# Kernel tuning notes

Measured on AMD Instinct MI355X. Metric: run time of the kernel, lower is better.

The kernel has to match this reference:

```python
import jax, jax.numpy as jnp
import numpy as np

B, C, P, H, W = 64, 2048, 4, 14, 14
HID = C * P // 2  # 4096
S = H * W         # 196


def setup_inputs() -> dict:
    key = jax.random.key(0)
    k1, k2, k3, k4, k5 = jax.random.split(key, 5)
    x = jax.random.normal(k1, (B, C, H, W), dtype=jnp.float32)
    w1 = jax.random.normal(k2, (HID, C), dtype=jnp.float32) * 0.02
    b1 = jnp.zeros((HID,), dtype=jnp.float32)
    w2 = jax.random.normal(k3, (C * P, HID), dtype=jnp.float32) * 0.02
    b2 = jnp.zeros((C * P,), dtype=jnp.float32)
    return {"x": x, "w1": w1, "b1": b1, "w2": w2, "b2": b2}


def reference(x, w1, b1, w2, b2):
    # SE-style gating: global average pool -> fc1 -> sigmoid -> fc2 -> sigmoid
    g = x.mean(axis=(2, 3))                                  # [B, C]
    h = jax.nn.sigmoid(g @ w1.T + b1)                        # [B, HID]
    w = jax.nn.sigmoid(h @ w2.T + b2).reshape(B, P, C)       # grouping_result [B, P, C]
    # Weighted feature: mean over channels of w[b,p,c] * x[b,c,s].
    # Original materializes [B,P,C,196] then AdaptiveAvgPool3d over C;
    # mathematically this is a batched matmul divided by C.
    xs = x.reshape(B, C, S)                                  # [B, C, 196]
    feat = jnp.einsum('bpc,bcs->bps', w, xs) / C             # [B, P, 196]
    return (w, feat.reshape(B, P, H, W))
```

## Files before the change

### kernel.cpp

```cpp
#include <hip/hip_runtime.h>
#include <hip/hip_bf16.h>
#include <cstdint>
#include <cstddef>

typedef __attribute__((ext_vector_type(4))) float  f32x4;
typedef __attribute__((ext_vector_type(8))) short  short8;

typedef __attribute__((address_space(3))) uint32_t as3_u32;
typedef __attribute__((address_space(1))) uint32_t as1_u32;

__device__ __forceinline__ short f2bf(float f) {
  __hip_bfloat16 h = __float2bfloat16(f);
  return *reinterpret_cast<short*>(&h);
}
__device__ __forceinline__ float sigmoidf(float x) {
  return 1.0f / (1.0f + __expf(-x));
}

__global__ __launch_bounds__(256) void pool_kernel(const float* __restrict__ x,
                                                   short* __restrict__ g) {
  __shared__ float sums[784];
  const int tid = threadIdx.x;
  const f32x4* base = (const f32x4*)(x + (size_t)blockIdx.x * (16 * 196));
#pragma unroll
  for (int it = 0; it < 4; ++it) {
    int i = it * 256 + tid;
    if (it < 3 || tid < 16) {
      f32x4 v = base[i];
      sums[i] = v[0] + v[1] + v[2] + v[3];
    }
  }
  __syncthreads();
  if (tid < 16) {
    float s = 0.f;
#pragma unroll
    for (int j = 0; j < 49; ++j) s += sums[tid * 49 + j];
    g[blockIdx.x * 16 + tid] = f2bf(s * (1.0f / 196.0f));
  }
}

template<int N, int K, int WAVES, bool OUT_BF16>
__device__ __forceinline__ void gemm_body(const short* __restrict__ A,
                                          const float* __restrict__ B,
                                          const float* __restrict__ bias,
                                          void* __restrict__ outp,
                                          float* __restrict__ red) {
  constexpr int KW = K / WAVES;
  constexpr int NK = KW / 32;
  constexpr int NT = WAVES * 64;
  const int n0  = blockIdx.x * 16;
  const int tid = threadIdx.x;
  const int l   = tid & 63;
  const int wv  = tid >> 6;
  const int kw0 = wv * KW;

  const int ko = (l >> 4) * 8;
  const float* Bp = B + (size_t)(n0 + (l & 15)) * K + kw0 + ko;
  const short* Ap = A + (size_t)(l & 15) * K + kw0 + ko;

  f32x4 acc0 = {}, acc1 = {}, acc2 = {}, acc3 = {};

  f32x4 bc0 = *(const f32x4*)(Bp);
  f32x4 bc1 = *(const f32x4*)(Bp + 4);
  short8 ac0 = *(const short8*)(Ap);
  short8 ac1 = *(const short8*)(Ap + 16 * K);
  short8 ac2 = *(const short8*)(Ap + 32 * K);
  short8 ac3 = *(const short8*)(Ap + 48 * K);

  for (int t = 0; t < NK; ++t) {
    f32x4 bn0 = {}, bn1 = {};
    short8 an0 = {}, an1 = {}, an2 = {}, an3 = {};
    if (t + 1 < NK) {
      const float* bp = Bp + (t + 1) * 32;
      const short* ap = Ap + (t + 1) * 32;
      bn0 = *(const f32x4*)(bp);
      bn1 = *(const f32x4*)(bp + 4);
      an0 = *(const short8*)(ap);
      an1 = *(const short8*)(ap + 16 * K);
      an2 = *(const short8*)(ap + 32 * K);
      an3 = *(const short8*)(ap + 48 * K);
    }
    short8 bb;
    bb[0] = f2bf(bc0[0]); bb[1] = f2bf(bc0[1]); bb[2] = f2bf(bc0[2]); bb[3] = f2bf(bc0[3]);
    bb[4] = f2bf(bc1[0]); bb[5] = f2bf(bc1[1]); bb[6] = f2bf(bc1[2]); bb[7] = f2bf(bc1[3]);
    acc0 = __builtin_amdgcn_mfma_f32_16x16x32_bf16(ac0, bb, acc0, 0, 0, 0);
    acc1 = __builtin_amdgcn_mfma_f32_16x16x32_bf16(ac1, bb, acc1, 0, 0, 0);
    acc2 = __builtin_amdgcn_mfma_f32_16x16x32_bf16(ac2, bb, acc2, 0, 0, 0);
    acc3 = __builtin_amdgcn_mfma_f32_16x16x32_bf16(ac3, bb, acc3, 0, 0, 0);
    bc0 = bn0; bc1 = bn1;
    ac0 = an0; ac1 = an1; ac2 = an2; ac3 = an3;
  }

  {
    float* rw = red + wv * 1024;
    const int mb = (l >> 4) << 2;
    const int nn = l & 15;
#pragma unroll
    for (int r = 0; r < 4; ++r) rw[(0  + mb + r) * 16 + nn] = acc0[r];
#pragma unroll
    for (int r = 0; r < 4; ++r) rw[(16 + mb + r) * 16 + nn] = acc1[r];
#pragma unroll
    for (int r = 0; r < 4; ++r) rw[(32 + mb + r) * 16 + nn] = acc2[r];
#pragma unroll
    for (int r = 0; r < 4; ++r) rw[(48 + mb + r) * 16 + nn] = acc3[r];
  }
  __syncthreads();

#pragma unroll
  for (int i = tid; i < 1024; i += NT) {
    float s = 0.f;
#pragma unroll
    for (int w = 0; w < WAVES; ++w) s += red[w * 1024 + i];
    int m  = i >> 4;
    int nn = n0 + (i & 15);
    s = sigmoidf(s + bias[nn]);
    if constexpr (OUT_BF16) ((short*)outp)[(size_t)m * N + nn] = f2bf(s);
    else                    ((float*)outp)[(size_t)m * N + nn] = s;
  }
}

__global__ __launch_bounds__(1024, 4) void gemm1_kernel(const short* __restrict__ A,
                                                        const float* __restrict__ B,
                                                        const float* __restrict__ bias,
                                                        short* __restrict__ outp) {
  __shared__ float red[16 * 1024];
  gemm_body<4096, 2048, 16, true>(A, B, bias, outp, red);
}

__global__ __launch_bounds__(512, 4) void gemm2_kernel(const short* __restrict__ A,
                                                       const float* __restrict__ B,
                                                       const float* __restrict__ bias,
                                                       float* __restrict__ outp,
                                                       float* __restrict__ zbuf) {
  constexpr int N = 8192, K = 4096;
  __shared__ float lds[16384];
  const int tid = threadIdx.x;
  const int l   = tid & 63;
  const int wv  = tid >> 6;
  const int n0  = blockIdx.x * 16;

  if (tid < 98) zbuf[blockIdx.x * 98 + tid] = 0.f;

  const char*  gB = (const char*)B + (size_t)n0 * (K * 4);
  const short* Ap = A + (size_t)(l & 15) * K + ((l >> 4) << 3);

  f32x4 acc0 = {}, acc1 = {}, acc2 = {}, acc3 = {};
  short8 a_cur[8], a_nxt[8];

#define G2_STAGE(c_, buf_)                                                     \
  {                                                                            \
    _Pragma("unroll")                                                          \
    for (int j = 0; j < 4; ++j) {                                              \
      int idx = j * 512 + tid;                                                 \
      int r   = idx >> 7;                                                      \
      int d   = (idx & 127) << 4;                                              \
      int s   = d ^ ((r & 7) << 4);                                            \
      const char* src = gB + (size_t)r * (K * 4) + (size_t)(c_) * 2048 + s;    \
      char* dst = (char*)lds + (buf_) * 32768 +                                \
                  (size_t)(j * 512 + (tid & ~63)) * 16;                        \
      __builtin_amdgcn_global_load_lds((as1_u32*)src, (as3_u32*)dst, 16, 0, 0);\
    }                                                                          \
  }
#define G2_LOADA(c_, ar_)                                                      \
  {                                                                            \
    const short* ap = Ap + (c_) * 512 + wv * 64;                               \
    _Pragma("unroll")                                                          \
    for (int t = 0; t < 2; ++t) {                                              \
      _Pragma("unroll")                                                        \
      for (int f = 0; f < 4; ++f)                                              \
        ar_[t * 4 + f] = *(const short8*)(ap + t * 32 + (size_t)f * 16 * K);   \
    }                                                                          \
  }

  G2_LOADA(0, a_cur);
  G2_STAGE(0, 0);
  __syncthreads();

  const int row = l & 15;
  const int swz = (row & 7) << 4;
  const int rb  = row * 2048;
  const int ko4 = ((l >> 4) << 3) << 2;

  for (int c = 0; c < 8; ++c) {
    if (c < 7) {
      G2_LOADA(c + 1, a_nxt);
      G2_STAGE(c + 1, (c + 1) & 1);
    }
    const char* bufc = (const char*)lds + (c & 1) * 32768;
#pragma unroll
    for (int t = 0; t < 2; ++t) {
      int kb = (wv << 8) + (t << 7) + ko4;
      f32x4 b0 = *(const f32x4*)(bufc + rb + ((kb)      ^ swz));
      f32x4 b1 = *(const f32x4*)(bufc + rb + ((kb + 16) ^ swz));
      short8 bb;
      bb[0] = f2bf(b0[0]); bb[1] = f2bf(b0[1]); bb[2] = f2bf(b0[2]); bb[3] = f2bf(b0[3]);
      bb[4] = f2bf(b1[0]); bb[5] = f2bf(b1[1]); bb[6] = f2bf(b1[2]); bb[7] = f2bf(b1[3]);
      acc0 = __builtin_amdgcn_mfma_f32_16x16x32_bf16(a_cur[t * 4 + 0], bb, acc0, 0, 0, 0);
      acc1 = __builtin_amdgcn_mfma_f32_16x16x32_bf16(a_cur[t * 4 + 1], bb, acc1, 0, 0, 0);
      acc2 = __builtin_amdgcn_mfma_f32_16x16x32_bf16(a_cur[t * 4 + 2], bb, acc2, 0, 0, 0);
      acc3 = __builtin_amdgcn_mfma_f32_16x16x32_bf16(a_cur[t * 4 + 3], bb, acc3, 0, 0, 0);
    }
    __syncthreads();
    if (c < 7) {
#pragma unroll
      for (int i = 0; i < 8; ++i) a_cur[i] = a_nxt[i];
    }
  }

  float* red = lds;
  {
    float* rw = red + wv * 1024;
    const int mb = (l >> 4) << 2;
    const int nn = l & 15;
#pragma unroll
    for (int r = 0; r < 4; ++r) rw[(0  + mb + r) * 16 + nn] = acc0[r];
#pragma unroll
    for (int r = 0; r < 4; ++r) rw[(16 + mb + r) * 16 + nn] = acc1[r];
#pragma unroll
    for (int r = 0; r < 4; ++r) rw[(32 + mb + r) * 16 + nn] = acc2[r];
#pragma unroll
    for (int r = 0; r < 4; ++r) rw[(48 + mb + r) * 16 + nn] = acc3[r];
  }
  __syncthreads();
#pragma unroll
  for (int i = tid; i < 1024; i += 512) {
    float s = 0.f;
#pragma unroll
    for (int w = 0; w < 8; ++w) s += red[w * 1024 + i];
    int m  = i >> 4;
    int nn = n0 + (i & 15);
    outp[(size_t)m * N + nn] = sigmoidf(s + bias[nn]);
  }
#undef G2_STAGE
#undef G2_LOADA
}

__global__ __launch_bounds__(256) void einsum_kernel(const float* __restrict__ x,
                                                     const float* __restrict__ wg,
                                                     float* __restrict__ feat) {
  const int b   = blockIdx.x >> 4;
  const int cc  = blockIdx.x & 15;
  const int tid = threadIdx.x;
  if (tid >= 196) return;
  const float* wp = wg + (size_t)b * 8192 + cc * 128;
  const float* xp = x + (size_t)b * 2048 * 196 + (size_t)cc * 128 * 196 + tid;
  float a0 = 0.f, a1 = 0.f, a2 = 0.f, a3 = 0.f;
#pragma unroll 8
  for (int c = 0; c < 128; ++c) {
    float xv = xp[(size_t)c * 196];
    a0 = __builtin_fmaf(wp[c],        xv, a0);
    a1 = __builtin_fmaf(wp[2048 + c], xv, a1);
    a2 = __builtin_fmaf(wp[4096 + c], xv, a2);
    a3 = __builtin_fmaf(wp[6144 + c], xv, a3);
  }
  const float invC = 1.0f / 2048.0f;
  atomicAdd(feat + (b * 4 + 0) * 196 + tid, a0 * invC);
  atomicAdd(feat + (b * 4 + 1) * 196 + tid, a1 * invC);
  atomicAdd(feat + (b * 4 + 2) * 196 + tid, a2 * invC);
  atomicAdd(feat + (b * 4 + 3) * 196 + tid, a3 * invC);
}

extern "C" void kernel_launch(void* const* d_in, const int* in_sizes, int n_in,
                              void* d_out, int out_size, void* d_ws, size_t ws_size,
                              hipStream_t stream) {
  const float* x  = (const float*)d_in[0];
  const float* w1 = (const float*)d_in[1];
  const float* b1 = (const float*)d_in[2];
  const float* w2 = (const float*)d_in[3];
  const float* b2 = (const float*)d_in[4];
  float* out = (float*)d_out;

  short* g_bf = (short*)d_ws;
  short* h_bf = g_bf + 64 * 2048;

  float* wout = out;
  float* feat = out + 524288;

  pool_kernel<<<8192, 256, 0, stream>>>(x, g_bf);

  gemm1_kernel<<<4096 / 16, 1024, 0, stream>>>(g_bf, w1, b1, h_bf);

  gemm2_kernel<<<512, 512, 0, stream>>>(h_bf, w2, b2, wout, feat);

  einsum_kernel<<<64 * 16, 256, 0, stream>>>(x, wout, feat);
}
```

Baseline: 96.37 us.

## Triple-buffer gemm2 B tiles with smaller K chunks and explicit vmcnt waits

Restructures the gemm2 main loop from 8 double-buffered 512-wide K chunks to 16 triple-buffered 256-wide chunks. It uses manual s_waitcnt vmcnt and raw s_barrier with sched_barriers, so two stages stay in flight while computing. LDS use drops to 48KB and the launch bound rises to 6 blocks per CU, aiming for more loads in flight and higher occupancy. The cost is more loop iterations and barriers, and hand-tuned wait counts that must exactly match the number of issued loads.

```diff
diff --git a/kernel.cpp b/kernel.cpp
--- a/kernel.cpp
+++ b/kernel.cpp
@@ -127,13 +127,13 @@
   gemm_body<4096, 2048, 16, true>(A, B, bias, outp, red);
 }
 
-__global__ __launch_bounds__(512, 4) void gemm2_kernel(const short* __restrict__ A,
+__global__ __launch_bounds__(512, 6) void gemm2_kernel(const short* __restrict__ A,
                                                        const float* __restrict__ B,
                                                        const float* __restrict__ bias,
                                                        float* __restrict__ outp,
                                                        float* __restrict__ zbuf) {
   constexpr int N = 8192, K = 4096;
-  __shared__ float lds[16384];
+  __shared__ float lds[12288];
   const int tid = threadIdx.x;
   const int l   = tid & 63;
   const int wv  = tid >> 6;
@@ -144,69 +144,76 @@
   const char*  gB = (const char*)B + (size_t)n0 * (K * 4);
   const short* Ap = A + (size_t)(l & 15) * K + ((l >> 4) << 3);
 
-  f32x4 acc0 = {}, acc1 = {}, acc2 = {}, acc3 = {};
-  short8 a_cur[8], a_nxt[8];
-
-#define G2_STAGE(c_, buf_)                                                     \
+#define G2_STAGE(c_, b_)                                                       \
   {                                                                            \
     _Pragma("unroll")                                                          \
-    for (int j = 0; j < 4; ++j) {                                              \
+    for (int j = 0; j < 2; ++j) {                                              \
       int idx = j * 512 + tid;                                                 \
-      int r   = idx >> 7;                                                      \
-      int d   = (idx & 127) << 4;                                              \
+      int r   = idx >> 6;                                                      \
+      int d   = (idx & 63) << 4;                                               \
       int s   = d ^ ((r & 7) << 4);                                            \
-      const char* src = gB + (size_t)r * (K * 4) + (size_t)(c_) * 2048 + s;    \
-      char* dst = (char*)lds + (buf_) * 32768 +                                \
+      const char* src = gB + (size_t)r * (K * 4) + (size_t)(c_) * 1024 + s;    \
+      char* dst = (char*)lds + (size_t)(b_) * 16384 +                          \
                   (size_t)(j * 512 + (tid & ~63)) * 16;                        \
       __builtin_amdgcn_global_load_lds((as1_u32*)src, (as3_u32*)dst, 16, 0, 0);\
     }                                                                          \
   }
 #define G2_LOADA(c_, ar_)                                                      \
   {                                                                            \
-    const short* ap = Ap + (c_) * 512 + wv * 64;                               \
+    const short* ap = Ap + (c_) * 256 + wv * 32;                               \
     _Pragma("unroll")                                                          \
-    for (int t = 0; t < 2; ++t) {                                              \
-      _Pragma("unroll")                                                        \
-      for (int f = 0; f < 4; ++f)                                              \
-        ar_[t * 4 + f] = *(const short8*)(ap + t * 32 + (size_t)f * 16 * K);   \
-    }                                                                          \
-  }
-
-  G2_LOADA(0, a_cur);
+    for (int f = 0; f < 4; ++f)                                                \
+      ar_[f] = *(const short8*)(ap + (size_t)f * 16 * K);                      \
+  }
+
+  f32x4 acc0 = {}, acc1 = {}, acc2 = {}, acc3 = {};
+  short8 aC[4], aN[4];
+
   G2_STAGE(0, 0);
-  __syncthreads();
+  __builtin_amdgcn_sched_barrier(0);
+  G2_LOADA(0, aC);
+  __builtin_amdgcn_sched_barrier(0);
+  G2_STAGE(1, 1);
+  __builtin_amdgcn_sched_barrier(0);
 
   const int row = l & 15;
   const int swz = (row & 7) << 4;
-  const int rb  = row * 2048;
-  const int ko4 = ((l >> 4) << 3) << 2;
-
-  for (int c = 0; c < 8; ++c) {
-    if (c < 7) {
-      G2_LOADA(c + 1, a_nxt);
-      G2_STAGE(c + 1, (c + 1) & 1);
+  const int rb  = row * 1024;
+  const int kb  = (wv << 7) + ((l >> 4) << 5);
+
+  int s0i = 0, s1i = 1, s2i = 2;
+
+#pragma unroll 1
+  for (int c = 0; c < 16; ++c) {
+    if (c < 15) { asm volatile("s_waitcnt vmcnt(6)" ::: "memory"); }
+    else        { asm volatile("s_waitcnt vmcnt(4)" ::: "memory"); }
+    __builtin_amdgcn_sched_barrier(0);
+    __builtin_amdgcn_s_barrier();
+    __builtin_amdgcn_sched_barrier(0);
+    if (c + 1 < 16) { G2_LOADA(c + 1, aN); }
+    __builtin_amdgcn_sched_barrier(0);
+    if (c + 2 < 16) { G2_STAGE(c + 2, s2i); }
+    __builtin_amdgcn_sched_barrier(0);
+
+    const char* bufc = (const char*)lds + (size_t)s0i * 16384;
+    f32x4 b0 = *(const f32x4*)(bufc + rb + ((kb)      ^ swz));
+    f32x4 b1 = *(const f32x4*)(bufc + rb + ((kb + 16) ^ swz));
+    short8 bb;
+    bb[0] = f2bf(b0[0]); bb[1] = f2bf(b0[1]); bb[2] = f2bf(b0[2]); bb[3] = f2bf(b0[3]);
+    bb[4] = f2bf(b1[0]); bb[5] = f2bf(b1[1]); bb[6] = f2bf(b1[2]); bb[7] = f2bf(b1[3]);
+    acc0 = __builtin_amdgcn_mfma_f32_16x16x32_bf16(aC[0], bb, acc0, 0, 0, 0);
+    acc1 = __builtin_amdgcn_mfma_f32_16x16x32_bf16(aC[1], bb, acc1, 0, 0, 0);
+    acc2 = __builtin_amdgcn_mfma_f32_16x16x32_bf16(aC[2], bb, acc2, 0, 0, 0);
+    acc3 = __builtin_amdgcn_mfma_f32_16x16x32_bf16(aC[3], bb, acc3, 0, 0, 0);
+
+    if (c + 1 < 16) {
+#pragma unroll
+      for (int f = 0; f < 4; ++f) aC[f] = aN[f];
     }
-    const char* bufc = (const char*)lds + (c & 1) * 32768;
-#pragma unroll
-    for (int t = 0; t < 2; ++t) {
-      int kb = (wv << 8) + (t << 7) + ko4;
-      f32x4 b0 = *(const f32x4*)(bufc + rb + ((kb)      ^ swz));
-      f32x4 b1 = *(const f32x4*)(bufc + rb + ((kb + 16) ^ swz));
-      short8 bb;
-      bb[0] = f2bf(b0[0]); bb[1] = f2bf(b0[1]); bb[2] = f2bf(b0[2]); bb[3] = f2bf(b0[3]);
-      bb[4] = f2bf(b1[0]); bb[5] = f2bf(b1[1]); bb[6] = f2bf(b1[2]); bb[7] = f2bf(b1[3]);
-      acc0 = __builtin_amdgcn_mfma_f32_16x16x32_bf16(a_cur[t * 4 + 0], bb, acc0, 0, 0, 0);
-      acc1 = __builtin_amdgcn_mfma_f32_16x16x32_bf16(a_cur[t * 4 + 1], bb, acc1, 0, 0, 0);
-      acc2 = __builtin_amdgcn_mfma_f32_16x16x32_bf16(a_cur[t * 4 + 2], bb, acc2, 0, 0, 0);
-      acc3 = __builtin_amdgcn_mfma_f32_16x16x32_bf16(a_cur[t * 4 + 3], bb, acc3, 0, 0, 0);
-    }
-    __syncthreads();
-    if (c < 7) {
-#pragma unroll
-      for (int i = 0; i < 8; ++i) a_cur[i] = a_nxt[i];
-    }
-  }
-
+    int t = s0i; s0i = s1i; s1i = s2i; s2i = t;
+  }
+
+  __syncthreads();
   float* red = lds;
   {
     float* rw = red + wv * 1024;
```

New measurement: 94.96 us. No clear change (-1.5%).

## Stage W2 in two large half-K LDS chunks instead of double-buffered pipeline

Applied to the files above, without the earlier changes.

The gemm2 kernel stops using an 8-step double-buffered staging of W2 rows. It now loads half of K (128 KB of LDS) per chunk in two steps, with a sync before and after each load, and software-pipelines the A fragment loads within a chunk. The aim is fewer barriers and larger in-flight global-to-LDS transfers. The cost is that each load is no longer overlapped with compute, and the 128 KB LDS footprint limits occupancy to one block per CU (launch bounds min-blocks removed). Other edits are cosmetic (nn computation, pool grid expressed as an expression).

```diff
diff --git a/kernel.cpp b/kernel.cpp
--- a/kernel.cpp
+++ b/kernel.cpp
@@ -112,7 +112,8 @@
 #pragma unroll
     for (int w = 0; w < WAVES; ++w) s += red[w * 1024 + i];
     int m  = i >> 4;
-    int nn = n0 + (i & 15);
+    int nn = i & 15;
+    nn += n0;
     s = sigmoidf(s + bias[nn]);
     if constexpr (OUT_BF16) ((short*)outp)[(size_t)m * N + nn] = f2bf(s);
     else                    ((float*)outp)[(size_t)m * N + nn] = s;
@@ -127,13 +128,13 @@
   gemm_body<4096, 2048, 16, true>(A, B, bias, outp, red);
 }
 
-__global__ __launch_bounds__(512, 4) void gemm2_kernel(const short* __restrict__ A,
-                                                       const float* __restrict__ B,
-                                                       const float* __restrict__ bias,
-                                                       float* __restrict__ outp,
-                                                       float* __restrict__ zbuf) {
+__global__ __launch_bounds__(512) void gemm2_kernel(const short* __restrict__ A,
+                                                    const float* __restrict__ B,
+                                                    const float* __restrict__ bias,
+                                                    float* __restrict__ outp,
+                                                    float* __restrict__ zbuf) {
   constexpr int N = 8192, K = 4096;
-  __shared__ float lds[16384];
+  __shared__ char ldsb[131072];
   const int tid = threadIdx.x;
   const int l   = tid & 63;
   const int wv  = tid >> 6;
@@ -145,69 +146,56 @@
   const short* Ap = A + (size_t)(l & 15) * K + ((l >> 4) << 3);
 
   f32x4 acc0 = {}, acc1 = {}, acc2 = {}, acc3 = {};
-  short8 a_cur[8], a_nxt[8];
-
-#define G2_STAGE(c_, buf_)                                                     \
-  {                                                                            \
-    _Pragma("unroll")                                                          \
-    for (int j = 0; j < 4; ++j) {                                              \
-      int idx = j * 512 + tid;                                                 \
-      int r   = idx >> 7;                                                      \
-      int d   = (idx & 127) << 4;                                              \
-      int s   = d ^ ((r & 7) << 4);                                            \
-      const char* src = gB + (size_t)r * (K * 4) + (size_t)(c_) * 2048 + s;    \
-      char* dst = (char*)lds + (buf_) * 32768 +                                \
-                  (size_t)(j * 512 + (tid & ~63)) * 16;                        \
-      __builtin_amdgcn_global_load_lds((as1_u32*)src, (as3_u32*)dst, 16, 0, 0);\
-    }                                                                          \
-  }
-#define G2_LOADA(c_, ar_)                                                      \
-  {                                                                            \
-    const short* ap = Ap + (c_) * 512 + wv * 64;                               \
-    _Pragma("unroll")                                                          \
-    for (int t = 0; t < 2; ++t) {                                              \
-      _Pragma("unroll")                                                        \
-      for (int f = 0; f < 4; ++f)                                              \
-        ar_[t * 4 + f] = *(const short8*)(ap + t * 32 + (size_t)f * 16 * K);   \
-    }                                                                          \
-  }
-
-  G2_LOADA(0, a_cur);
-  G2_STAGE(0, 0);
-  __syncthreads();
 
   const int row = l & 15;
   const int swz = (row & 7) << 4;
-  const int rb  = row * 2048;
-  const int ko4 = ((l >> 4) << 3) << 2;
-
-  for (int c = 0; c < 8; ++c) {
-    if (c < 7) {
-      G2_LOADA(c + 1, a_nxt);
-      G2_STAGE(c + 1, (c + 1) & 1);
-    }
-    const char* bufc = (const char*)lds + (c & 1) * 32768;
-#pragma unroll
-    for (int t = 0; t < 2; ++t) {
-      int kb = (wv << 8) + (t << 7) + ko4;
-      f32x4 b0 = *(const f32x4*)(bufc + rb + ((kb)      ^ swz));
-      f32x4 b1 = *(const f32x4*)(bufc + rb + ((kb + 16) ^ swz));
+  const int rb  = row * 8192;
+  const int dsw = tid * 16;
+  const int dstu = (tid & ~63) * 16;
+
+#pragma unroll 1
+  for (int ch = 0; ch < 2; ++ch) {
+    __syncthreads();
+#pragma unroll
+    for (int j = 0; j < 16; ++j) {
+      const char* src = gB + (size_t)j * (K * 4) + (size_t)ch * 8192
+                           + (dsw ^ ((j & 7) << 4));
+      char* dst = ldsb + j * 8192 + dstu;
+      __builtin_amdgcn_global_load_lds((as1_u32*)src, (as3_u32*)dst, 16, 0, 0);
+    }
+    __syncthreads();
+
+    const short* ap0 = Ap + ch * 2048 + wv * 256;
+    short8 aC0 = *(const short8*)(ap0);
+    short8 aC1 = *(const short8*)(ap0 + 16 * K);
+    short8 aC2 = *(const short8*)(ap0 + 32 * K);
+    short8 aC3 = *(const short8*)(ap0 + 48 * K);
+#pragma unroll
+    for (int t = 0; t < 8; ++t) {
+      short8 aN0 = {}, aN1 = {}, aN2 = {}, aN3 = {};
+      if (t + 1 < 8) {
+        const short* ap = ap0 + (t + 1) * 32;
+        aN0 = *(const short8*)(ap);
+        aN1 = *(const short8*)(ap + 16 * K);
+        aN2 = *(const short8*)(ap + 32 * K);
+        aN3 = *(const short8*)(ap + 48 * K);
+      }
+      const int koff = (wv << 10) + (t << 7) + ((l >> 4) << 5);
+      f32x4 b0 = *(const f32x4*)(ldsb + rb + ((koff)      ^ swz));
+      f32x4 b1 = *(const f32x4*)(ldsb + rb + ((koff + 16) ^ swz));
       short8 bb;
       bb[0] = f2bf(b0[0]); bb[1] = f2bf(b0[1]); bb[2] = f2bf(b0[2]); bb[3] = f2bf(b0[3]);
       bb[4] = f2bf(b1[0]); bb[5] = f2bf(b1[1]); bb[6] = f2bf(b1[2]); bb[7] = f2bf(b1[3]);
-      acc0 = __builtin_amdgcn_mfma_f32_16x16x32_bf16(a_cur[t * 4 + 0], bb, acc0, 0, 0, 0);
-      acc1 = __builtin_amdgcn_mfma_f32_16x16x32_bf16(a_cur[t * 4 + 1], bb, acc1, 0, 0, 0);
-      acc2 = __builtin_amdgcn_mfma_f32_16x16x32_bf16(a_cur[t * 4 + 2], bb, acc2, 0, 0, 0);
-      acc3 = __builtin_amdgcn_mfma_f32_16x16x32_bf16(a_cur[t * 4 + 3], bb, acc3, 0, 0, 0);
-    }
-    __syncthreads();
-    if (c < 7) {
-#pragma unroll
-      for (int i = 0; i < 8; ++i) a_cur[i] = a_nxt[i];
-    }
-  }
-
-  float* red = lds;
+      acc0 = __builtin_amdgcn_mfma_f32_16x16x32_bf16(aC0, bb, acc0, 0, 0, 0);
+      acc1 = __builtin_amdgcn_mfma_f32_16x16x32_bf16(aC1, bb, acc1, 0, 0, 0);
+      acc2 = __builtin_amdgcn_mfma_f32_16x16x32_bf16(aC2, bb, acc2, 0, 0, 0);
+      acc3 = __builtin_amdgcn_mfma_f32_16x16x32_bf16(aC3, bb, acc3, 0, 0, 0);
+      aC0 = aN0; aC1 = aN1; aC2 = aN2; aC3 = aN3;
+    }
+  }
+
+  __syncthreads();
+  float* red = (float*)ldsb;
   {
     float* rw = red + wv * 1024;
     const int mb = (l >> 4) << 2;
@@ -231,8 +219,6 @@
     int nn = n0 + (i & 15);
     outp[(size_t)m * N + nn] = sigmoidf(s + bias[nn]);
   }
-#undef G2_STAGE
-#undef G2_LOADA
 }
 
 __global__ __launch_bounds__(256) void einsum_kernel(const float* __restrict__ x,
@@ -276,7 +262,7 @@
   float* wout = out;
   float* feat = out + 524288;
 
-  pool_kernel<<<8192, 256, 0, stream>>>(x, g_bf);
+  pool_kernel<<<(64 * 2048) / 16, 256, 0, stream>>>(x, g_bf);
 
   gemm1_kernel<<<4096 / 16, 1024, 0, stream>>>(g_bf, w1, b1, h_bf);
 
```

Result: slower. 103.5 us (+7.4%).
